# Optimization experiments

Hardware: AMD Instinct MI355X
Metric: run time of the kernel (lower is better)

The kernel has to match this reference:

```python
import jax, jax.numpy as jnp
import numpy as np

BS, SEQ, NUM_SKILLS, DIM_S, SIZE_M = 64, 200, 4096, 256, 64

def setup_inputs():
    key = jax.random.key(0)
    ks = jax.random.split(key, 16)
    def n(k, shape, s=0.05):
        return jax.random.normal(k, shape, dtype=jnp.float32) * s
    return {
        "q": jax.random.randint(ks[0], (BS, SEQ), 0, NUM_SKILLS),
        "r": jax.random.randint(ks[1], (BS, SEQ), 0, 2),
        "k_emb": n(ks[2], (NUM_SKILLS, DIM_S)),
        "x_emb": n(ks[3], (2 * NUM_SKILLS + 1, DIM_S)),
        "Mk": n(ks[4], (SIZE_M, DIM_S)),
        "Mv0": n(ks[5], (SIZE_M, DIM_S)),
        "W_a": n(ks[6], (DIM_S, 2 * DIM_S)), "b_a": jnp.zeros((DIM_S,), jnp.float32),
        "W_e": n(ks[7], (DIM_S, DIM_S)), "b_e": jnp.zeros((DIM_S,), jnp.float32),
        "W_add": n(ks[8], (DIM_S, DIM_S)), "b_add": jnp.zeros((DIM_S,), jnp.float32),
        "W_f": n(ks[9], (DIM_S, 2 * DIM_S)), "b_f": jnp.zeros((DIM_S,), jnp.float32),
        "hx": n(ks[10], (1, DIM_S)), "cx": n(ks[11], (1, DIM_S)),
        "W_ih": n(ks[12], (4 * DIM_S, DIM_S)), "b_ih": jnp.zeros((4 * DIM_S,), jnp.float32),
        "W_hh": n(ks[13], (4 * DIM_S, DIM_S)), "b_hh": jnp.zeros((4 * DIM_S,), jnp.float32),
        "W_p": n(ks[14], (1, DIM_S)), "b_p": jnp.zeros((1,), jnp.float32),
    }

def _forward(q, r, k_emb, x_emb, Mk, Mv0, W_a, b_a, W_e, b_e, W_add, b_add,
             W_f, b_f, hx, cx, W_ih, b_ih, W_hh, b_hh, W_p, b_p):
    num_skills = k_emb.shape[0]
    bs = q.shape[0]
    k = k_emb[q]                                    # (bs, seq, d) question key embedding
    v = x_emb[q + num_skills * r]                   # (bs, seq, d) interaction embedding
    # DKVMN addressing against the static key memory Mk (precomputable for all t)
    w = jax.nn.softmax(jnp.einsum('bsd,md->bsm', k, Mk), axis=-1)
    # write control input: a_embed(cat(k, v)), then erase/add head projections
    we = jnp.einsum('bse,de->bsd', jnp.concatenate([k, v], axis=-1), W_a) + b_a
    erase = jax.nn.sigmoid(jnp.einsum('bsd,ed->bse', we, W_e) + b_e)
    add = jnp.tanh(jnp.einsum('bsd,ed->bse', we, W_add) + b_add)
    mem0 = jnp.broadcast_to(Mv0, (bs,) + Mv0.shape)  # (bs, m, d)

    def mem_step(mem, inp):
        wt, et, at = inp                             # (bs,m), (bs,d), (bs,d)
        read = jnp.einsum('bm,bmd->bd', wt, mem)     # weighted read BEFORE write
        ww = wt[:, :, None]
        mem = mem * (1.0 - ww * et[:, None, :]) + ww * at[:, None, :]
        return mem, read

    _, reads = jax.lax.scan(mem_step, mem0,
                            (w.transpose(1, 0, 2), erase.transpose(1, 0, 2), add.transpose(1, 0, 2)))
    reads = reads.transpose(1, 0, 2)                 # (bs, seq, d)
    f = jnp.tanh(jnp.einsum('bse,de->bsd', jnp.concatenate([reads, k], axis=-1), W_f) + b_f)

    def lstm_step(carry, ft):
        h, c = carry
        gates = ft @ W_ih.T + b_ih + h @ W_hh.T + b_hh
        i_g, f_g, g_g, o_g = jnp.split(gates, 4, axis=-1)  # torch LSTMCell gate order
        c = jax.nn.sigmoid(f_g) * c + jax.nn.sigmoid(i_g) * jnp.tanh(g_g)
        h = jax.nn.sigmoid(o_g) * jnp.tanh(c)
        return (h, c), h

    d = hx.shape[1]
    h0 = jnp.broadcast_to(hx, (bs, d))
    c0 = jnp.broadcast_to(cx, (bs, d))
    _, hs = jax.lax.scan(lstm_step, (h0, c0), f.transpose(1, 0, 2))
    hs = hs.transpose(1, 0, 2)                       # (bs, seq, d)
    p = jax.nn.sigmoid(jnp.einsum('bsd,od->bso', hs, W_p) + b_p)[..., 0]
    return p                                         # (bs, seq)

def reference(q, r, k_emb, x_emb, Mk, Mv0, W_a, b_a, W_e, b_e, W_add, b_add,
              W_f, b_f, hx, cx, W_ih, b_ih, W_hh, b_hh, W_p, b_p):
    return _forward(q, r, k_emb, x_emb, Mk, Mv0, W_a, b_a, W_e, b_e, W_add, b_add,
                    W_f, b_f, hx, cx, W_ih, b_ih, W_hh, b_hh, W_p, b_p)
```

## Files before the change

kernel.cpp:

```cpp
#include <hip/hip_runtime.h>
#include <hip/hip_bf16.h>

#define BS 64
#define SEQ 200
#define NSK 4096
#define DS 256
#define SM 64
#define NROWS (BS*SEQ)
#define LBLK 8

typedef __attribute__((ext_vector_type(8))) short bf16x8;
typedef __attribute__((ext_vector_type(4))) float f32x4;
typedef unsigned long long u64;

__device__ __forceinline__ float sigf(float x){ return 1.0f/(1.0f+expf(-x)); }
__device__ __forceinline__ float fast_sig(float x){ return 1.0f/(1.0f+__expf(-x)); }
__device__ __forceinline__ float fast_tanh(float x){
  float t = __expf(-2.0f*fabsf(x));
  float r = (1.0f - t)/(1.0f + t);
  return copysignf(r, x);
}
__device__ __forceinline__ short f2bf(float x){
  unsigned int u = __float_as_uint(x);
  unsigned int r = (u + 0x7fffu + ((u >> 16) & 1u)) >> 16;
  return (short)r;
}
__device__ __forceinline__ float bf2f(unsigned short s){
  return __uint_as_float(((unsigned int)s) << 16);
}

__global__ __launch_bounds__(256) void k_gather_attn(
    const int* __restrict__ q, const int* __restrict__ r,
    const float* __restrict__ k_emb, const float* __restrict__ x_emb,
    const float* __restrict__ Mk,
    float* __restrict__ X2, float* __restrict__ vbuf, float* __restrict__ wbuf)
{
  __shared__ float ks[4][DS];
  const int tid = threadIdx.x;
  const int wv = tid >> 6, ln = tid & 63;
  const int row = blockIdx.x * 4 + wv;
  const int b = row / SEQ, s = row % SEQ;
  const int qi = q[b*SEQ + s];
  const int ri = r[b*SEQ + s];
  const float4* kr = (const float4*)(k_emb + (size_t)qi * DS);
  const float4* vr = (const float4*)(x_emb + ((size_t)qi + (size_t)NSK * ri) * DS);
  float4 kv = kr[ln];
  float4 vv = vr[ln];
  ((float4*)(X2 + (size_t)row*512 + DS))[ln] = kv;
  ((float4*)(vbuf + (size_t)row*DS))[ln] = vv;
  *((float4*)&ks[wv][ln*4]) = kv;
  __syncthreads();
  const float4* mkr = (const float4*)(Mk + (size_t)ln * DS);
  float a0=0.f,a1=0.f,a2=0.f,a3=0.f;
  #pragma unroll 8
  for (int d4=0; d4<DS/4; d4++){
    float4 m4 = mkr[d4];
    float4 k4 = *((const float4*)&ks[wv][d4*4]);
    a0 += m4.x*k4.x; a1 += m4.y*k4.y; a2 += m4.z*k4.z; a3 += m4.w*k4.w;
  }
  float lg = (a0+a1)+(a2+a3);
  float mx = lg;
  #pragma unroll
  for (int off=32; off; off>>=1) mx = fmaxf(mx, __shfl_xor(mx, off));
  float ex = expf(lg - mx);
  float sm = ex;
  #pragma unroll
  for (int off=32; off; off>>=1) sm += __shfl_xor(sm, off);
  wbuf[(size_t)row*SM + ln] = ex / sm;
}

template<int ACT, int ABF, int OUT>
__global__ __launch_bounds__(256) void k_gemm2(
    const void* __restrict__ A0, int lda0, int K0,
    const void* __restrict__ A1, int lda1, int K1,
    const float* __restrict__ W, const float* __restrict__ bias,
    const float* __restrict__ bias2,
    void* __restrict__ C, int N)
{
  const int K = K0 + K1;
  __shared__ __align__(16) char As[64*80];
  __shared__ __align__(16) char Bs[64*80];
  const int tid = threadIdx.x;
  const int l = tid & 63, w = tid >> 6;
  const int m0 = blockIdx.x * 64, n0 = blockIdx.y * 64;
  const int mh = w >> 1, nh = w & 1;
  const int srow = tid >> 2, sseg = tid & 3;

  f32x4 acc[2][2];
  #pragma unroll
  for (int i=0;i<2;i++)
    #pragma unroll
    for (int j=0;j<2;j++) acc[i][j] = (f32x4){0.f,0.f,0.f,0.f};

  for (int k0=0; k0<K; k0+=32){
    const int kk = k0 + sseg*8;
    bf16x8 av;
    if (ABF){
      const ushort* ap = (kk < K0) ? (const ushort*)A0 + (size_t)(m0+srow)*lda0 + kk
                                   : (const ushort*)A1 + (size_t)(m0+srow)*lda1 + (kk-K0);
      av = *(const bf16x8*)ap;
    } else {
      const float* ap = (kk < K0) ? (const float*)A0 + (size_t)(m0+srow)*lda0 + kk
                                  : (const float*)A1 + (size_t)(m0+srow)*lda1 + (kk-K0);
      float4 a1 = *(const float4*)ap;
      float4 a2 = *(const float4*)(ap+4);
      av[0]=f2bf(a1.x); av[1]=f2bf(a1.y); av[2]=f2bf(a1.z); av[3]=f2bf(a1.w);
      av[4]=f2bf(a2.x); av[5]=f2bf(a2.y); av[6]=f2bf(a2.z); av[7]=f2bf(a2.w);
    }
    *(bf16x8*)(As + srow*80 + ((sseg ^ (srow&3))*16)) = av;
    const float* wp = W + (size_t)(n0+srow)*K + kk;
    float4 b1 = *(const float4*)wp;
    float4 b2 = *(const float4*)(wp+4);
    bf16x8 bv;
    bv[0]=f2bf(b1.x); bv[1]=f2bf(b1.y); bv[2]=f2bf(b1.z); bv[3]=f2bf(b1.w);
    bv[4]=f2bf(b2.x); bv[5]=f2bf(b2.y); bv[6]=f2bf(b2.z); bv[7]=f2bf(b2.w);
    *(bf16x8*)(Bs + srow*80 + ((sseg ^ (srow&3))*16)) = bv;
    __syncthreads();
    bf16x8 af[2], bf[2];
    #pragma unroll
    for (int mi=0; mi<2; mi++){
      const int row = mh*32 + mi*16 + (l&15);
      af[mi] = *(const bf16x8*)(As + row*80 + (((l>>4) ^ (row&3))*16));
    }
    #pragma unroll
    for (int ni=0; ni<2; ni++){
      const int row = nh*32 + ni*16 + (l&15);
      bf[ni] = *(const bf16x8*)(Bs + row*80 + (((l>>4) ^ (row&3))*16));
    }
    #pragma unroll
    for (int mi=0; mi<2; mi++)
      #pragma unroll
      for (int ni=0; ni<2; ni++)
        acc[mi][ni] = __builtin_amdgcn_mfma_f32_16x16x32_bf16(af[mi], bf[ni], acc[mi][ni], 0,0,0);
    __syncthreads();
  }
  #pragma unroll
  for (int mi=0; mi<2; mi++){
    #pragma unroll
    for (int ni=0; ni<2; ni++){
      const int n = n0 + nh*32 + ni*16 + (l&15);
      float bsum = bias[n] + (bias2 ? bias2[n] : 0.f);
      #pragma unroll
      for (int j=0;j<4;j++){
        const int m = m0 + mh*32 + mi*16 + (l>>4)*4 + j;
        float v = acc[mi][ni][j] + bsum;
        if (ACT==1) v = sigf(v);
        else if (ACT==2) v = tanhf(v);
        if (OUT==0)      ((float*)C)[(size_t)m*N + n] = v;
        else if (OUT==1) ((ushort*)C)[(size_t)m*N + n] = (ushort)f2bf(v);
        else             ((ushort*)C)[(size_t)m*N + ((n&255)*4 + (n>>8))] = (ushort)f2bf(v);
      }
    }
  }
}

__global__ __launch_bounds__(256) void k_gemm_ea(
    const ushort* __restrict__ A, const float* __restrict__ W_e,
    const float* __restrict__ b_e, const float* __restrict__ W_add,
    const float* __restrict__ b_add,
    float* __restrict__ ebuf, float* __restrict__ abuf)
{
  __shared__ __align__(16) char As[64*80];
  __shared__ __align__(16) char Bse[64*80];
  __shared__ __align__(16) char Bsa[64*80];
  const int tid = threadIdx.x;
  const int l = tid & 63, w = tid >> 6;
  const int m0 = blockIdx.x * 64, n0 = blockIdx.y * 64;
  const int mh = w >> 1, nh = w & 1;
  const int srow = tid >> 2, sseg = tid & 3;

  f32x4 acce[2][2], acca[2][2];
  #pragma unroll
  for (int i=0;i<2;i++)
    #pragma unroll
    for (int j=0;j<2;j++){ acce[i][j]=(f32x4){0.f,0.f,0.f,0.f}; acca[i][j]=(f32x4){0.f,0.f,0.f,0.f}; }

  for (int k0=0; k0<DS; k0+=32){
    const int kk = k0 + sseg*8;
    bf16x8 av = *(const bf16x8*)(A + (size_t)(m0+srow)*DS + kk);
    *(bf16x8*)(As + srow*80 + ((sseg ^ (srow&3))*16)) = av;
    {
      const float* wp = W_e + (size_t)(n0+srow)*DS + kk;
      float4 b1 = *(const float4*)wp; float4 b2 = *(const float4*)(wp+4);
      bf16x8 bv;
      bv[0]=f2bf(b1.x); bv[1]=f2bf(b1.y); bv[2]=f2bf(b1.z); bv[3]=f2bf(b1.w);
      bv[4]=f2bf(b2.x); bv[5]=f2bf(b2.y); bv[6]=f2bf(b2.z); bv[7]=f2bf(b2.w);
      *(bf16x8*)(Bse + srow*80 + ((sseg ^ (srow&3))*16)) = bv;
    }
    {
      const float* wp = W_add + (size_t)(n0+srow)*DS + kk;
      float4 b1 = *(const float4*)wp; float4 b2 = *(const float4*)(wp+4);
      bf16x8 bv;
      bv[0]=f2bf(b1.x); bv[1]=f2bf(b1.y); bv[2]=f2bf(b1.z); bv[3]=f2bf(b1.w);
      bv[4]=f2bf(b2.x); bv[5]=f2bf(b2.y); bv[6]=f2bf(b2.z); bv[7]=f2bf(b2.w);
      *(bf16x8*)(Bsa + srow*80 + ((sseg ^ (srow&3))*16)) = bv;
    }
    __syncthreads();
    bf16x8 af[2], bfe[2], bfa[2];
    #pragma unroll
    for (int mi=0; mi<2; mi++){
      const int row = mh*32 + mi*16 + (l&15);
      af[mi] = *(const bf16x8*)(As + row*80 + (((l>>4) ^ (row&3))*16));
    }
    #pragma unroll
    for (int ni=0; ni<2; ni++){
      const int row = nh*32 + ni*16 + (l&15);
      bfe[ni] = *(const bf16x8*)(Bse + row*80 + (((l>>4) ^ (row&3))*16));
      bfa[ni] = *(const bf16x8*)(Bsa + row*80 + (((l>>4) ^ (row&3))*16));
    }
    #pragma unroll
    for (int mi=0; mi<2; mi++)
      #pragma unroll
      for (int ni=0; ni<2; ni++){
        acce[mi][ni] = __builtin_amdgcn_mfma_f32_16x16x32_bf16(af[mi], bfe[ni], acce[mi][ni], 0,0,0);
        acca[mi][ni] = __builtin_amdgcn_mfma_f32_16x16x32_bf16(af[mi], bfa[ni], acca[mi][ni], 0,0,0);
      }
    __syncthreads();
  }
  #pragma unroll
  for (int mi=0; mi<2; mi++){
    #pragma unroll
    for (int ni=0; ni<2; ni++){
      const int n = n0 + nh*32 + ni*16 + (l&15);
      const float be = b_e[n], ba = b_add[n];
      #pragma unroll
      for (int j=0;j<4;j++){
        const int m = m0 + mh*32 + mi*16 + (l>>4)*4 + j;
        ebuf[(size_t)m*DS + n] = sigf(acce[mi][ni][j] + be);
        abuf[(size_t)m*DS + n] = tanhf(acca[mi][ni][j] + ba);
      }
    }
  }
}

__global__ __launch_bounds__(256) void k_scan(
    const float* __restrict__ wbuf, const float* __restrict__ ebuf,
    const float* __restrict__ abuf, const float* __restrict__ Mv0,
    float* __restrict__ X2)
{
  const int b = blockIdx.x;
  const int d = threadIdx.x;
  __shared__ float ws[SM];
  float mem[SM];
  #pragma unroll
  for (int m=0;m<SM;m++) mem[m] = Mv0[m*DS + d];
  for (int t=0;t<SEQ;t++){
    const size_t row = (size_t)b*SEQ + t;
    if (d < SM) ws[d] = wbuf[row*SM + d];
    const float e = ebuf[row*DS + d];
    const float a = abuf[row*DS + d];
    __syncthreads();
    float r0=0.f,r1=0.f,r2=0.f,r3=0.f;
    #pragma unroll
    for (int m=0;m<SM;m+=4){
      float w0=ws[m], w1=ws[m+1], w2=ws[m+2], w3=ws[m+3];
      r0 += w0*mem[m];   mem[m]   += w0*fmaf(-e, mem[m],   a);
      r1 += w1*mem[m+1]; mem[m+1] += w1*fmaf(-e, mem[m+1], a);
      r2 += w2*mem[m+2]; mem[m+2] += w2*fmaf(-e, mem[m+2], a);
      r3 += w3*mem[m+3]; mem[m+3] += w3*fmaf(-e, mem[m+3], a);
    }
    X2[row*512 + d] = (r0+r1)+(r2+r3);
    __syncthreads();
  }
}

__global__ __launch_bounds__(512, 2) void k_lstm2(
    const ushort* __restrict__ gin2, const float* __restrict__ W_hh,
    const float* __restrict__ hx, const float* __restrict__ cx,
    short* __restrict__ hhist, unsigned long long* __restrict__ xbuf)
{
  const int bb = blockIdx.x;
  const int p  = bb >> 1;
  const int ro = bb & 1;
  const int tid = threadIdx.x;
  const int l   = tid & 63;
  const int w   = tid >> 6;

  __shared__ short hsm[2][16*256];

  bf16x8 wfr[4][8];
  {
    const int col  = l & 15;
    const int krow = (l >> 4) * 8;
    #pragma unroll
    for (int gt=0; gt<4; gt++){
      const int G = gt*256 + ro*128 + w*16 + col;
      const float* wrow = W_hh + (size_t)G*256;
      #pragma unroll
      for (int kt=0; kt<8; kt++){
        const int k0 = kt*32 + krow;
        float4 wa = *(const float4*)(wrow + k0);
        float4 wb = *(const float4*)(wrow + k0 + 4);
        bf16x8 f;
        f[0]=f2bf(wa.x); f[1]=f2bf(wa.y); f[2]=f2bf(wa.z); f[3]=f2bf(wa.w);
        f[4]=f2bf(wb.x); f[5]=f2bf(wb.y); f[6]=f2bf(wb.z); f[7]=f2bf(wb.w);
        wfr[gt][kt] = f;
      }
    }
  }

  const int dhalf = w*16 + (l & 15);
  const int gdim  = ro*128 + dhalf;
  float c_[4];
  {
    float c0 = cx[gdim];
    #pragma unroll
    for (int r=0;r<4;r++) c_[r] = c0;
  }

  if (tid < 256){
    const int row = tid >> 4, seg = tid & 15;
    #pragma unroll
    for (int u=0; u<2; u++){
      const int kb = seg*32 + u*16;
      const int d0 = kb >> 1;
      float4 ha = *(const float4*)(hx + d0);
      float4 hb = *(const float4*)(hx + d0 + 4);
      bf16x8 v;
      v[0]=f2bf(ha.x); v[1]=f2bf(ha.y); v[2]=f2bf(ha.z); v[3]=f2bf(ha.w);
      v[4]=f2bf(hb.x); v[5]=f2bf(hb.y); v[6]=f2bf(hb.z); v[7]=f2bf(hb.w);
      *(bf16x8*)((char*)hsm[0] + row*512 + (kb ^ ((row&7)<<4))) = v;
    }
  }

  u64 gpre[4];
  #pragma unroll
  for (int r=0; r<4; r++){
    const int b = p*16 + (l>>4)*4 + r;
    gpre[r] = *(const u64*)(gin2 + ((size_t)(b*SEQ))*1024 + gdim*4);
  }

  unsigned long long* myslots = xbuf + (size_t)(p*2 + ro)*1024;
  unsigned long long* pslots  = xbuf + (size_t)(p*2 + (1-ro))*1024;

  for (int t=0; t<SEQ; t++){
    __syncthreads();
    const int cur = t & 1;

    f32x4 acc[4];
    #pragma unroll
    for (int gt=0; gt<4; gt++) acc[gt] = (f32x4){0.f,0.f,0.f,0.f};
    const int r0 = l & 15;
    #pragma unroll
    for (int kt=0; kt<8; kt++){
      const int kbyte = kt*64 + (l>>4)*16;
      bf16x8 a = *(const bf16x8*)((const char*)hsm[cur] + r0*512 + (kbyte ^ ((r0&7)<<4)));
      #pragma unroll
      for (int gt=0; gt<4; gt++)
        acc[gt] = __builtin_amdgcn_mfma_f32_16x16x32_bf16(a, wfr[gt][kt], acc[gt], 0,0,0);
    }

    const unsigned int tag = (unsigned int)(t + 1);
    #pragma unroll
    for (int r=0; r<4; r++){
      const int bat = (l>>4)*4 + r;
      const int b = p*16 + bat;
      const u64 gv = gpre[r];
      float iv = acc[0][r] + bf2f((unsigned short)(gv       & 0xffffu));
      float fv = acc[1][r] + bf2f((unsigned short)((gv>>16) & 0xffffu));
      float gg = acc[2][r] + bf2f((unsigned short)((gv>>32) & 0xffffu));
      float ov = acc[3][r] + bf2f((unsigned short)((gv>>48) & 0xffffu));
      float cc = fast_sig(fv)*c_[r] + fast_sig(iv)*fast_tanh(gg);
      c_[r] = cc;
      float h = fast_sig(ov)*fast_tanh(cc);
      unsigned short hb = (unsigned short)f2bf(h);
      hhist[((size_t)(b*SEQ + t))*256 + gdim] = (short)hb;
      *(short*)((char*)hsm[cur^1] + bat*512 + ((gdim*2) ^ ((bat&7)<<4))) = (short)hb;
      unsigned short nb = (unsigned short)__shfl_xor((int)hb, 1);
      if ((l & 1) == 0){
        unsigned long long v = ((unsigned long long)hb << 48)
                             | ((unsigned long long)nb << 32)
                             | (unsigned long long)tag;
        __hip_atomic_store(&myslots[bat*64 + (dhalf>>1)], v,
                           __ATOMIC_RELAXED, __HIP_MEMORY_SCOPE_AGENT);
      }
    }

    if (t == SEQ-1) break;

    #pragma unroll
    for (int r=0; r<4; r++){
      const int b = p*16 + (l>>4)*4 + r;
      gpre[r] = *(const u64*)(gin2 + ((size_t)(b*SEQ + t+1))*1024 + gdim*4);
    }

    {
      const int s0 = tid*2, s1 = tid*2 + 1;
      unsigned long long v0=0, v1=0;
      bool ok0=false, ok1=false;
      while (true){
        if (!ok0){ v0 = __hip_atomic_load(&pslots[s0], __ATOMIC_RELAXED, __HIP_MEMORY_SCOPE_AGENT);
                   ok0 = ((unsigned int)v0 == tag); }
        if (!ok1){ v1 = __hip_atomic_load(&pslots[s1], __ATOMIC_RELAXED, __HIP_MEMORY_SCOPE_AGENT);
                   ok1 = ((unsigned int)v1 == tag); }
        if (ok0 && ok1) break;
        __builtin_amdgcn_s_sleep(1);
      }
      #pragma unroll
      for (int u=0; u<2; u++){
        unsigned long long v = u ? v1 : v0;
        const int sid = u ? s1 : s0;
        const int bat = sid >> 6;
        const int dp  = sid & 63;
        const int dpart = (1-ro)*128 + dp*2;
        unsigned int wv = (unsigned int)((v >> 48) & 0xffffu)
                        | (((unsigned int)(v >> 32) & 0xffffu) << 16);
        *(unsigned int*)((char*)hsm[cur^1] + bat*512 + ((dpart*2) ^ ((bat&7)<<4))) = wv;
      }
    }
  }
}

__global__ __launch_bounds__(256) void k_pout(
    const short* __restrict__ hhist, const float* __restrict__ W_p,
    const float* __restrict__ b_p, float* __restrict__ out)
{
  const int tid = threadIdx.x;
  const int row = blockIdx.x*4 + (tid>>6);
  const int ln = tid & 63;
  ushort4 hv = ((const ushort4*)(hhist + (size_t)row*256))[ln];
  float4 wp = ((const float4*)W_p)[ln];
  float s = bf2f(hv.x)*wp.x + bf2f(hv.y)*wp.y + bf2f(hv.z)*wp.z + bf2f(hv.w)*wp.w;
  #pragma unroll
  for (int off=32; off; off>>=1) s += __shfl_xor(s, off);
  if (ln == 0) out[row] = sigf(s + b_p[0]);
}

extern "C" void kernel_launch(void* const* d_in, const int* in_sizes, int n_in,
                              void* d_out, int out_size, void* d_ws, size_t ws_size,
                              hipStream_t stream)
{
  const int*   q     = (const int*)d_in[0];
  const int*   r     = (const int*)d_in[1];
  const float* k_emb = (const float*)d_in[2];
  const float* x_emb = (const float*)d_in[3];
  const float* Mk    = (const float*)d_in[4];
  const float* Mv0   = (const float*)d_in[5];
  const float* W_a   = (const float*)d_in[6];
  const float* b_a   = (const float*)d_in[7];
  const float* W_e   = (const float*)d_in[8];
  const float* b_e   = (const float*)d_in[9];
  const float* W_add = (const float*)d_in[10];
  const float* b_add = (const float*)d_in[11];
  const float* W_f   = (const float*)d_in[12];
  const float* b_f   = (const float*)d_in[13];
  const float* hx    = (const float*)d_in[14];
  const float* cx    = (const float*)d_in[15];
  const float* W_ih  = (const float*)d_in[16];
  const float* b_ih  = (const float*)d_in[17];
  const float* W_hh  = (const float*)d_in[18];
  const float* b_hh  = (const float*)d_in[19];
  const float* W_p   = (const float*)d_in[20];
  const float* b_p   = (const float*)d_in[21];
  float* out = (float*)d_out;

  char* base = (char*)d_ws;
  float*  vbuf  = (float*)(base);
  ushort* webuf = (ushort*)(base + 13107200);
  float*  ebuf  = (float*)(base + 19660800);
  float*  abuf  = (float*)(base + 32768000);
  float*  X2    = (float*)(base + 45875200);
  float*  wbuf  = (float*)(base + 72089600);
  ushort* fbuf  = (ushort*)(base + 75366400);
  ushort* gin2  = (ushort*)(base);
  short*  hhist = (short*)fbuf;
  unsigned long long* xbuf = (unsigned long long*)(base + 81920000);

  k_gather_attn<<<NROWS/4, 256, 0, stream>>>(q, r, k_emb, x_emb, Mk, X2, vbuf, wbuf);
  k_gemm2<0,0,1><<<dim3(NROWS/64, 4), 256, 0, stream>>>(X2+DS, 512, DS, vbuf, DS, DS, W_a, b_a, nullptr, webuf, DS);
  k_gemm_ea<<<dim3(NROWS/64, 4), 256, 0, stream>>>(webuf, W_e, b_e, W_add, b_add, ebuf, abuf);
  k_scan<<<BS, DS, 0, stream>>>(wbuf, ebuf, abuf, Mv0, X2);
  k_gemm2<2,0,1><<<dim3(NROWS/64, 4), 256, 0, stream>>>(X2, 512, DS, X2+DS, 512, DS, W_f, b_f, nullptr, fbuf, DS);
  k_gemm2<0,1,2><<<dim3(NROWS/64, 16), 256, 0, stream>>>(fbuf, DS, DS, fbuf, DS, 0, W_ih, b_ih, b_hh, gin2, 1024);
  {
    const ushort* gin_c = gin2;
    void* args[] = { (void*)&gin_c, (void*)&W_hh, (void*)&hx, (void*)&cx,
                     (void*)&hhist, (void*)&xbuf };
    hipLaunchCooperativeKernel((void*)k_lstm2, dim3(LBLK), dim3(512), args, 0, stream);
  }
  k_pout<<<NROWS/4, 256, 0, stream>>>(hhist, W_p, b_p, out);
}
```

Measured before the change: 1.039 ms.

## Pre-convert weights to bf16, widen W_ih GEMM N-tile, prefetch scan inputs

Adds a kernel that converts W_a, W_e, W_add, W_f and W_ih to bf16 once per call, so the GEMM kernels load bf16 weights directly and no longer convert fp32 to bf16 per tile. k_gemm2 gains an NT template parameter, and the W_ih projection now uses two 64-column B tiles per block to reuse the A tile and halve the grid. The memory scan kernel register-prefetches the next timestep's w, e and a values before the update loop to hide global load latency on the sequential path. The cost is an extra kernel launch, a workspace region, and more registers and shared memory in the NT=2 GEMM.

```diff
diff --git a/kernel.cpp b/kernel.cpp
--- a/kernel.cpp
+++ b/kernel.cpp
@@ -27,6 +27,27 @@
 }
 __device__ __forceinline__ float bf2f(unsigned short s){
   return __uint_as_float(((unsigned int)s) << 16);
+}
+
+__global__ __launch_bounds__(256) void k_cvtw(
+    const float* __restrict__ Wa, const float* __restrict__ We,
+    const float* __restrict__ Wadd, const float* __restrict__ Wf,
+    const float* __restrict__ Wih, ushort* __restrict__ out)
+{
+  const int bid = blockIdx.x;
+  const float* src; size_t rbase; int lb;
+  if      (bid < 64) { src = Wa;   rbase = 0;      lb = bid; }
+  else if (bid < 96) { src = We;   rbase = 131072; lb = bid - 64; }
+  else if (bid < 128){ src = Wadd; rbase = 196608; lb = bid - 96; }
+  else if (bid < 192){ src = Wf;   rbase = 262144; lb = bid - 128; }
+  else               { src = Wih;  rbase = 393216; lb = bid - 192; }
+  const int idx = (lb*256 + threadIdx.x) * 8;
+  float4 a1 = *(const float4*)(src + idx);
+  float4 a2 = *(const float4*)(src + idx + 4);
+  bf16x8 v;
+  v[0]=f2bf(a1.x); v[1]=f2bf(a1.y); v[2]=f2bf(a1.z); v[3]=f2bf(a1.w);
+  v[4]=f2bf(a2.x); v[5]=f2bf(a2.y); v[6]=f2bf(a2.z); v[7]=f2bf(a2.w);
+  *(bf16x8*)(out + rbase + idx) = v;
 }
 
 __global__ __launch_bounds__(256) void k_gather_attn(
@@ -69,28 +90,30 @@
   wbuf[(size_t)row*SM + ln] = ex / sm;
 }
 
-template<int ACT, int ABF, int OUT>
+template<int ACT, int ABF, int OUT, int NT>
 __global__ __launch_bounds__(256) void k_gemm2(
     const void* __restrict__ A0, int lda0, int K0,
     const void* __restrict__ A1, int lda1, int K1,
-    const float* __restrict__ W, const float* __restrict__ bias,
+    const ushort* __restrict__ W, const float* __restrict__ bias,
     const float* __restrict__ bias2,
     void* __restrict__ C, int N)
 {
   const int K = K0 + K1;
   __shared__ __align__(16) char As[64*80];
-  __shared__ __align__(16) char Bs[64*80];
+  __shared__ __align__(16) char Bs[NT][64*80];
   const int tid = threadIdx.x;
   const int l = tid & 63, w = tid >> 6;
-  const int m0 = blockIdx.x * 64, n0 = blockIdx.y * 64;
+  const int m0 = blockIdx.x * 64, n0 = blockIdx.y * (64*NT);
   const int mh = w >> 1, nh = w & 1;
   const int srow = tid >> 2, sseg = tid & 3;
 
-  f32x4 acc[2][2];
-  #pragma unroll
-  for (int i=0;i<2;i++)
-    #pragma unroll
-    for (int j=0;j<2;j++) acc[i][j] = (f32x4){0.f,0.f,0.f,0.f};
+  f32x4 acc[NT][2][2];
+  #pragma unroll
+  for (int nt=0; nt<NT; nt++)
+    #pragma unroll
+    for (int i=0;i<2;i++)
+      #pragma unroll
+      for (int j=0;j<2;j++) acc[nt][i][j] = (f32x4){0.f,0.f,0.f,0.f};
 
   for (int k0=0; k0<K; k0+=32){
     const int kk = k0 + sseg*8;
@@ -108,55 +131,60 @@
       av[4]=f2bf(a2.x); av[5]=f2bf(a2.y); av[6]=f2bf(a2.z); av[7]=f2bf(a2.w);
     }
     *(bf16x8*)(As + srow*80 + ((sseg ^ (srow&3))*16)) = av;
-    const float* wp = W + (size_t)(n0+srow)*K + kk;
-    float4 b1 = *(const float4*)wp;
-    float4 b2 = *(const float4*)(wp+4);
-    bf16x8 bv;
-    bv[0]=f2bf(b1.x); bv[1]=f2bf(b1.y); bv[2]=f2bf(b1.z); bv[3]=f2bf(b1.w);
-    bv[4]=f2bf(b2.x); bv[5]=f2bf(b2.y); bv[6]=f2bf(b2.z); bv[7]=f2bf(b2.w);
-    *(bf16x8*)(Bs + srow*80 + ((sseg ^ (srow&3))*16)) = bv;
-    __syncthreads();
-    bf16x8 af[2], bf[2];
+    #pragma unroll
+    for (int nt=0; nt<NT; nt++){
+      bf16x8 bv = *(const bf16x8*)(W + (size_t)(n0 + nt*64 + srow)*K + kk);
+      *(bf16x8*)(Bs[nt] + srow*80 + ((sseg ^ (srow&3))*16)) = bv;
+    }
+    __syncthreads();
+    bf16x8 af[2];
     #pragma unroll
     for (int mi=0; mi<2; mi++){
       const int row = mh*32 + mi*16 + (l&15);
       af[mi] = *(const bf16x8*)(As + row*80 + (((l>>4) ^ (row&3))*16));
     }
     #pragma unroll
-    for (int ni=0; ni<2; ni++){
-      const int row = nh*32 + ni*16 + (l&15);
-      bf[ni] = *(const bf16x8*)(Bs + row*80 + (((l>>4) ^ (row&3))*16));
-    }
-    #pragma unroll
-    for (int mi=0; mi<2; mi++)
-      #pragma unroll
-      for (int ni=0; ni<2; ni++)
-        acc[mi][ni] = __builtin_amdgcn_mfma_f32_16x16x32_bf16(af[mi], bf[ni], acc[mi][ni], 0,0,0);
-    __syncthreads();
-  }
-  #pragma unroll
-  for (int mi=0; mi<2; mi++){
-    #pragma unroll
-    for (int ni=0; ni<2; ni++){
-      const int n = n0 + nh*32 + ni*16 + (l&15);
-      float bsum = bias[n] + (bias2 ? bias2[n] : 0.f);
-      #pragma unroll
-      for (int j=0;j<4;j++){
-        const int m = m0 + mh*32 + mi*16 + (l>>4)*4 + j;
-        float v = acc[mi][ni][j] + bsum;
-        if (ACT==1) v = sigf(v);
-        else if (ACT==2) v = tanhf(v);
-        if (OUT==0)      ((float*)C)[(size_t)m*N + n] = v;
-        else if (OUT==1) ((ushort*)C)[(size_t)m*N + n] = (ushort)f2bf(v);
-        else             ((ushort*)C)[(size_t)m*N + ((n&255)*4 + (n>>8))] = (ushort)f2bf(v);
+    for (int nt=0; nt<NT; nt++){
+      bf16x8 bf[2];
+      #pragma unroll
+      for (int ni=0; ni<2; ni++){
+        const int row = nh*32 + ni*16 + (l&15);
+        bf[ni] = *(const bf16x8*)(Bs[nt] + row*80 + (((l>>4) ^ (row&3))*16));
+      }
+      #pragma unroll
+      for (int mi=0; mi<2; mi++)
+        #pragma unroll
+        for (int ni=0; ni<2; ni++)
+          acc[nt][mi][ni] = __builtin_amdgcn_mfma_f32_16x16x32_bf16(af[mi], bf[ni], acc[nt][mi][ni], 0,0,0);
+    }
+    __syncthreads();
+  }
+  #pragma unroll
+  for (int nt=0; nt<NT; nt++){
+    #pragma unroll
+    for (int mi=0; mi<2; mi++){
+      #pragma unroll
+      for (int ni=0; ni<2; ni++){
+        const int n = n0 + nt*64 + nh*32 + ni*16 + (l&15);
+        float bsum = bias[n] + (bias2 ? bias2[n] : 0.f);
+        #pragma unroll
+        for (int j=0;j<4;j++){
+          const int m = m0 + mh*32 + mi*16 + (l>>4)*4 + j;
+          float v = acc[nt][mi][ni][j] + bsum;
+          if (ACT==1) v = sigf(v);
+          else if (ACT==2) v = tanhf(v);
+          if (OUT==0)      ((float*)C)[(size_t)m*N + n] = v;
+          else if (OUT==1) ((ushort*)C)[(size_t)m*N + n] = (ushort)f2bf(v);
+          else             ((ushort*)C)[(size_t)m*N + ((n&255)*4 + (n>>8))] = (ushort)f2bf(v);
+        }
       }
     }
   }
 }
 
 __global__ __launch_bounds__(256) void k_gemm_ea(
-    const ushort* __restrict__ A, const float* __restrict__ W_e,
-    const float* __restrict__ b_e, const float* __restrict__ W_add,
+    const ushort* __restrict__ A, const ushort* __restrict__ We_bf,
+    const float* __restrict__ b_e, const ushort* __restrict__ Wadd_bf,
     const float* __restrict__ b_add,
     float* __restrict__ ebuf, float* __restrict__ abuf)
 {
@@ -179,22 +207,10 @@
     const int kk = k0 + sseg*8;
     bf16x8 av = *(const bf16x8*)(A + (size_t)(m0+srow)*DS + kk);
     *(bf16x8*)(As + srow*80 + ((sseg ^ (srow&3))*16)) = av;
-    {
-      const float* wp = W_e + (size_t)(n0+srow)*DS + kk;
-      float4 b1 = *(const float4*)wp; float4 b2 = *(const float4*)(wp+4);
-      bf16x8 bv;
-      bv[0]=f2bf(b1.x); bv[1]=f2bf(b1.y); bv[2]=f2bf(b1.z); bv[3]=f2bf(b1.w);
-      bv[4]=f2bf(b2.x); bv[5]=f2bf(b2.y); bv[6]=f2bf(b2.z); bv[7]=f2bf(b2.w);
-      *(bf16x8*)(Bse + srow*80 + ((sseg ^ (srow&3))*16)) = bv;
-    }
-    {
-      const float* wp = W_add + (size_t)(n0+srow)*DS + kk;
-      float4 b1 = *(const float4*)wp; float4 b2 = *(const float4*)(wp+4);
-      bf16x8 bv;
-      bv[0]=f2bf(b1.x); bv[1]=f2bf(b1.y); bv[2]=f2bf(b1.z); bv[3]=f2bf(b1.w);
-      bv[4]=f2bf(b2.x); bv[5]=f2bf(b2.y); bv[6]=f2bf(b2.z); bv[7]=f2bf(b2.w);
-      *(bf16x8*)(Bsa + srow*80 + ((sseg ^ (srow&3))*16)) = bv;
-    }
+    bf16x8 be = *(const bf16x8*)(We_bf + (size_t)(n0+srow)*DS + kk);
+    *(bf16x8*)(Bse + srow*80 + ((sseg ^ (srow&3))*16)) = be;
+    bf16x8 ba = *(const bf16x8*)(Wadd_bf + (size_t)(n0+srow)*DS + kk);
+    *(bf16x8*)(Bsa + srow*80 + ((sseg ^ (srow&3))*16)) = ba;
     __syncthreads();
     bf16x8 af[2], bfe[2], bfa[2];
     #pragma unroll
@@ -244,12 +260,19 @@
   float mem[SM];
   #pragma unroll
   for (int m=0;m<SM;m++) mem[m] = Mv0[m*DS + d];
+  const size_t rb = (size_t)b*SEQ;
+  float wn = (d < SM) ? wbuf[rb*SM + d] : 0.f;
+  float en = ebuf[rb*DS + d];
+  float an = abuf[rb*DS + d];
   for (int t=0;t<SEQ;t++){
-    const size_t row = (size_t)b*SEQ + t;
-    if (d < SM) ws[d] = wbuf[row*SM + d];
-    const float e = ebuf[row*DS + d];
-    const float a = abuf[row*DS + d];
-    __syncthreads();
+    if (d < SM) ws[d] = wn;
+    const float e = en, a = an;
+    __syncthreads();
+    if (t+1 < SEQ){
+      wn = (d < SM) ? wbuf[(rb+t+1)*SM + d] : 0.f;
+      en = ebuf[(rb+t+1)*DS + d];
+      an = abuf[(rb+t+1)*DS + d];
+    }
     float r0=0.f,r1=0.f,r2=0.f,r3=0.f;
     #pragma unroll
     for (int m=0;m<SM;m+=4){
@@ -259,7 +282,7 @@
       r2 += w2*mem[m+2]; mem[m+2] += w2*fmaf(-e, mem[m+2], a);
       r3 += w3*mem[m+3]; mem[m+3] += w3*fmaf(-e, mem[m+3], a);
     }
-    X2[row*512 + d] = (r0+r1)+(r2+r3);
+    X2[(rb+t)*512 + d] = (r0+r1)+(r2+r3);
     __syncthreads();
   }
 }
@@ -464,14 +487,22 @@
   ushort* fbuf  = (ushort*)(base + 75366400);
   ushort* gin2  = (ushort*)(base);
   short*  hhist = (short*)fbuf;
-  unsigned long long* xbuf = (unsigned long long*)(base + 81920000);
-
+  u64*    xbuf  = (u64*)(base + 81920000);
+  ushort* wbf   = (ushort*)(base + 82000000);
+
+  ushort* wa_bf   = wbf;
+  ushort* we_bf   = wbf + 131072;
+  ushort* wadd_bf = wbf + 196608;
+  ushort* wf_bf   = wbf + 262144;
+  ushort* wih_bf  = wbf + 393216;
+
+  k_cvtw<<<320, 256, 0, stream>>>(W_a, W_e, W_add, W_f, W_ih, wbf);
   k_gather_attn<<<NROWS/4, 256, 0, stream>>>(q, r, k_emb, x_emb, Mk, X2, vbuf, wbuf);
-  k_gemm2<0,0,1><<<dim3(NROWS/64, 4), 256, 0, stream>>>(X2+DS, 512, DS, vbuf, DS, DS, W_a, b_a, nullptr, webuf, DS);
-  k_gemm_ea<<<dim3(NROWS/64, 4), 256, 0, stream>>>(webuf, W_e, b_e, W_add, b_add, ebuf, abuf);
+  k_gemm2<0,0,1,1><<<dim3(NROWS/64, 4), 256, 0, stream>>>(X2+DS, 512, DS, vbuf, DS, DS, wa_bf, b_a, nullptr, webuf, DS);
+  k_gemm_ea<<<dim3(NROWS/64, 4), 256, 0, stream>>>(webuf, we_bf, b_e, wadd_bf, b_add, ebuf, abuf);
   k_scan<<<BS, DS, 0, stream>>>(wbuf, ebuf, abuf, Mv0, X2);
-  k_gemm2<2,0,1><<<dim3(NROWS/64, 4), 256, 0, stream>>>(X2, 512, DS, X2+DS, 512, DS, W_f, b_f, nullptr, fbuf, DS);
-  k_gemm2<0,1,2><<<dim3(NROWS/64, 16), 256, 0, stream>>>(fbuf, DS, DS, fbuf, DS, 0, W_ih, b_ih, b_hh, gin2, 1024);
+  k_gemm2<2,0,1,1><<<dim3(NROWS/64, 4), 256, 0, stream>>>(X2, 512, DS, X2+DS, 512, DS, wf_bf, b_f, nullptr, fbuf, DS);
+  k_gemm2<0,1,2,2><<<dim3(NROWS/64, 8), 256, 0, stream>>>(fbuf, DS, DS, fbuf, DS, 0, wih_bf, b_ih, b_hh, gin2, 1024);
   {
     const ushort* gin_c = gin2;
     void* args[] = { (void*)&gin_c, (void*)&W_hh, (void*)&hx, (void*)&cx,
```

Result: slower. 1.064 ms (+2.4%).
